# Optimization experiments

Measured on AMD Instinct MI355X. Metric: run time of the kernel, lower is better.

Reference implementation:

```python
import jax, jax.numpy as jnp
import numpy as np

NU, NI, NR = 50000, 50000, 5   # users, items, rating levels
D, B, LS, LI = 64, 512, 32, 64 # embed_dim, batch, max social nbrs, max item hist
NEG = -1e9


def setup_inputs() -> dict:
    key = jax.random.key(0)
    ks = iter(jax.random.split(key, 64))
    def lin(din, dout):
        s = 1.0 / np.sqrt(din)
        return (jax.random.uniform(next(ks), (din, dout), minval=-s, maxval=s, dtype=jnp.float32),
                jax.random.uniform(next(ks), (dout,), minval=-s, maxval=s, dtype=jnp.float32))
    inp = {}
    inp['user_w'] = jax.random.normal(next(ks), (NU, D), dtype=jnp.float32) * 0.1
    inp['item_w'] = jax.random.normal(next(ks), (NI, D), dtype=jnp.float32) * 0.1
    inp['rating_w'] = jax.random.normal(next(ks), (NR, D), dtype=jnp.float32) * 0.1
    for name, din, dout in [('i_ln1', 2*D, D), ('i_ln2', D, D), ('i_ln3', 2*D, D),
                            ('i_att1', 2*D, D), ('i_att2', D, D), ('i_att3', D, 1),
                            ('s_ln1', D, D), ('s_ln2', 2*D, D), ('s_ln3', D, D),
                            ('s_att1', 2*D, D), ('s_att2', D, D), ('s_att3', D, 1)]:
        w, b = lin(din, dout)
        inp[name + '_w'] = w
        inp[name + '_b'] = b
    inp['nodes'] = jax.random.randint(next(ks), (B,), 0, NU)
    inp['social_hist'] = jax.random.randint(next(ks), (NU, LS), 0, NU)
    inp['social_mask'] = jax.random.bernoulli(next(ks), 0.5, (NU, LS)).at[:, 0].set(True)
    inp['item_hist'] = jax.random.randint(next(ks), (NU, LI), 0, NI)
    inp['rating_hist'] = jax.random.randint(next(ks), (NU, LI), 0, NR)
    inp['item_mask'] = jax.random.bernoulli(next(ks), 0.5, (NU, LI)).at[:, 0].set(True)
    return inp


def reference(user_w, item_w, rating_w,
              i_ln1_w, i_ln1_b, i_ln2_w, i_ln2_b, i_ln3_w, i_ln3_b,
              i_att1_w, i_att1_b, i_att2_w, i_att2_b, i_att3_w, i_att3_b,
              s_ln1_w, s_ln1_b, s_ln2_w, s_ln2_b, s_ln3_w, s_ln3_b,
              s_att1_w, s_att1_b, s_att2_w, s_att2_b, s_att3_w, s_att3_b,
              nodes, social_hist, social_mask, item_hist, rating_hist, item_mask):
    relu = jax.nn.relu

    def attn(x, w1, b1, w2, b2, w3, b3, mask):
        # x: [..., L, 2D] -> softmax weights over valid neighbors: [..., L]
        h = relu(x @ w1 + b1)
        h = relu(h @ w2 + b2)
        logit = (h @ w3 + b3)[..., 0]
        logit = jnp.where(mask, logit, NEG)
        return jax.nn.softmax(logit, axis=-1)

    def item_final(uids):
        # uids: any shape [...]; returns [..., D]  (Aggre_item.item_final)
        its, rts, m = item_hist[uids], rating_hist[uids], item_mask[uids]
        x = jnp.concatenate([item_w[its], rating_w[rts]], axis=-1)   # [...,LI,2D]
        x = relu(x @ i_ln1_w + i_ln1_b)                              # [...,LI,D]
        u = user_w[uids]                                             # [...,D]
        a_in = jnp.concatenate([x, jnp.broadcast_to(u[..., None, :], x.shape)], axis=-1)
        alpha = attn(a_in, i_att1_w, i_att1_b, i_att2_w, i_att2_b, i_att3_w, i_att3_b, m)
        hI = jnp.einsum('...l,...ld->...d', alpha, x)                # attention-weighted sum
        hI = relu(hI @ i_ln2_w + i_ln2_b)
        return relu(jnp.concatenate([u, hI], axis=-1) @ i_ln3_w + i_ln3_b)

    # item-space factor of query users
    hI_self = item_final(nodes)                                      # [B,D]
    # social aggregation: item_final over each user's social neighbors
    nbrs, nmask = social_hist[nodes], social_mask[nodes]             # [B,LS]
    hI_nb = item_final(nbrs)                                         # [B,LS,D]
    u = user_w[nodes]                                                # [B,D]
    b_in = jnp.concatenate([hI_nb, jnp.broadcast_to(u[:, None, :], hI_nb.shape)], axis=-1)
    beta = attn(b_in, s_att1_w, s_att1_b, s_att2_w, s_att2_b, s_att3_w, s_att3_b, nmask)
    hS = jnp.einsum('bl,bld->bd', beta, hI_nb)
    hS = relu(hS @ s_ln1_w + s_ln1_b)
    f = jnp.concatenate([hI_self, hS], axis=-1)
    f = relu(f @ s_ln2_w + s_ln2_b)
    return relu(f @ s_ln3_w + s_ln3_b)
```

## Files before the change

kernel.cpp:

```cpp
#include <hip/hip_runtime.h>
#include <math.h>


#define NII 50000
#define BB 512
#define LSS 32
#define NT 16896

typedef short short8 __attribute__((ext_vector_type(8)));
typedef float f32x4 __attribute__((ext_vector_type(4)));

static __device__ __forceinline__ bool mread(const void* p, long i, int mode) {
  if (mode == 0) return ((const int*)p)[i] != 0;
  if (mode == 2) return ((const float*)p)[i] != 0.0f;
  return ((const unsigned char*)p)[i] != 0;
}

static __device__ __forceinline__ float wsum(float v) {
#pragma unroll
  for (int s = 1; s < 64; s <<= 1) v += __shfl_xor(v, s);
  return v;
}
static __device__ __forceinline__ float wmax(float v) {
#pragma unroll
  for (int s = 1; s < 64; s <<= 1) v = fmaxf(v, __shfl_xor(v, s));
  return v;
}
static __device__ __forceinline__ float rsum16(float v) {
#pragma unroll
  for (int s = 1; s < 16; s <<= 1) v += __shfl_xor(v, s);
  return v;
}

static __device__ __forceinline__ short bf16rne(float f) {
  unsigned u = __float_as_uint(f);
  u = (u + 0x7FFFu + ((u >> 16) & 1u)) >> 16;
  return (short)u;
}
static __device__ __forceinline__ float bf16tof(short h) {
  return __uint_as_float(((unsigned)(unsigned short)h) << 16);
}

static __device__ __forceinline__ void wave_fence() {
  asm volatile("s_waitcnt lgkmcnt(0)" ::: "memory");
  __builtin_amdgcn_sched_barrier(0);
}

__global__ void setup_kernel(const unsigned int* __restrict__ sm,
                             int* __restrict__ flag,
                             const float* __restrict__ rating_w,
                             const float* __restrict__ w1,
                             const float* __restrict__ b1,
                             float* __restrict__ RW1g,
                             const float* __restrict__ A1w,
                             const float* __restrict__ A2w,
                             short* __restrict__ B1,
                             short* __restrict__ B2,
                             short* __restrict__ W1hi,
                             short* __restrict__ W1lo,
                             const int* __restrict__ nodes,
                             const int* __restrict__ social_hist,
                             int* __restrict__ counter,
                             int* __restrict__ list,
                             int* __restrict__ aUid) {
  const int tid = threadIdx.x;
  if (blockIdx.x == 0) {
    __shared__ int notInt, notFloat;
    if (tid == 0) { notInt = 0; notFloat = 0; }
    __syncthreads();
    int ni = 0, nf = 0;
    for (int i = tid; i < 4096; i += 256) {
      unsigned int x = sm[i];
      if (x > 1u) ni = 1;
      if (x != 0u && x != 0x3F800000u) nf = 1;
    }
    if (ni) atomicOr(&notInt, 1);
    if (nf) atomicOr(&notFloat, 1);
    __syncthreads();
    if (tid == 0) flag[0] = notInt ? (notFloat ? 1 : 2) : 0;
  } else if (blockIdx.x == 1) {
    for (int t = tid; t < 320; t += 256) {
      const int r = t >> 6, c = t & 63;
      float acc = b1[c];
      for (int k = 0; k < 64; ++k)
        acc = fmaf(rating_w[r * 64 + k], w1[(64 + k) * 64 + c], acc);
      RW1g[r * 64 + c] = acc;
    }
  } else if (blockIdx.x == 2) {
    for (int idx = tid; idx < 4096; idx += 256) {
      int e = idx & 7, g = idx >> 3;
      int l = g & 63, q = g >> 6;
      int kb = q >> 2, nb = q & 3;
      int k = kb * 32 + ((l >> 4) & 3) * 8 + e;
      int col = nb * 16 + (l & 15);
      B1[idx] = bf16rne(A1w[k * 64 + col]);
      B2[idx] = bf16rne(A2w[k * 64 + col]);
      float a = w1[k * 64 + col];
      short h = bf16rne(a);
      W1hi[idx] = h;
      W1lo[idx] = bf16rne(a - bf16tof(h));
    }
  } else {
    __shared__ int nI, nF;
    if (tid == 0) { nI = 0; nF = 0; }
    __syncthreads();
    int ni = 0, nf = 0;
    for (int i = tid; i < 4096; i += 256) {
      unsigned int x = sm[i];
      if (x > 1u) ni = 1;
      if (x != 0u && x != 0x3F800000u) nf = 1;
    }
    if (ni) atomicOr(&nI, 1);
    if (nf) atomicOr(&nF, 1);
    __syncthreads();
    const int mode = nI ? (nF ? 1 : 2) : 0;
    const int t = (blockIdx.x - 3) * 256 + tid;
    if (t < NT) {
      int uid;
      bool active;
      if (t < BB) {
        active = true;
        uid = nodes[t];
      } else {
        int nb = t - BB;
        int b = nb >> 5, l = nb & 31;
        long mi = (long)nodes[b] * LSS + l;
        active = mread((const void*)sm, mi, mode);
        uid = active ? social_hist[mi] : 0;
      }
      if (active) {
        int pos = atomicAdd(counter, 1);
        list[pos] = t;
        aUid[pos] = uid;
      }
    }
  }
}

__global__ __launch_bounds__(256, 2)
void mid_kernel(const float* __restrict__ item_w,
                const short* __restrict__ W1hi,
                const short* __restrict__ W1lo,
                short* __restrict__ xbase16,
                const float* __restrict__ user_w,
                const float* __restrict__ A1w, const float* __restrict__ A1b,
                const int* __restrict__ aUid, const int* __restrict__ nActp,
                float* __restrict__ uA1buf) {
  const int tid = threadIdx.x, lane = tid & 63, w = tid >> 6;
  if (blockIdx.x < 512) {
    const int l15 = lane & 15, lg4 = lane >> 4;
    short8 bh[8], bl[8];
#pragma unroll
    for (int q = 0; q < 8; ++q) {
      bh[q] = *(const short8*)(W1hi + (q * 64 + lane) * 8);
      bl[q] = *(const short8*)(W1lo + (q * 64 + lane) * 8);
    }
    const int wid = blockIdx.x * 4 + w;
    for (int tile = wid; tile < 3125; tile += 2048) {
      const long r0 = (long)tile * 16;
      const float* ap = item_w + (r0 + l15) * 64 + lg4 * 8;
      short8 ah[2], al[2];
#pragma unroll
      for (int kb = 0; kb < 2; ++kb) {
        const float4 a = *(const float4*)(ap + kb * 32);
        const float4 b = *(const float4*)(ap + kb * 32 + 4);
        float v[8] = {a.x, a.y, a.z, a.w, b.x, b.y, b.z, b.w};
        short8 hi, lo;
#pragma unroll
        for (int e = 0; e < 8; ++e) {
          short h = bf16rne(v[e]);
          hi[e] = h;
          lo[e] = bf16rne(v[e] - bf16tof(h));
        }
        ah[kb] = hi;
        al[kb] = lo;
      }
#pragma unroll
      for (int nb = 0; nb < 4; ++nb) {
        f32x4 acc = {0.0f, 0.0f, 0.0f, 0.0f};
        acc = __builtin_amdgcn_mfma_f32_16x16x32_bf16(ah[0], bh[0 * 4 + nb], acc, 0, 0, 0);
        acc = __builtin_amdgcn_mfma_f32_16x16x32_bf16(ah[1], bh[1 * 4 + nb], acc, 0, 0, 0);
        acc = __builtin_amdgcn_mfma_f32_16x16x32_bf16(ah[0], bl[0 * 4 + nb], acc, 0, 0, 0);
        acc = __builtin_amdgcn_mfma_f32_16x16x32_bf16(ah[1], bl[1 * 4 + nb], acc, 0, 0, 0);
        acc = __builtin_amdgcn_mfma_f32_16x16x32_bf16(al[0], bh[0 * 4 + nb], acc, 0, 0, 0);
        acc = __builtin_amdgcn_mfma_f32_16x16x32_bf16(al[1], bh[1 * 4 + nb], acc, 0, 0, 0);
#pragma unroll
        for (int r = 0; r < 4; ++r)
          xbase16[(r0 + lg4 * 4 + r) * 64 + nb * 16 + l15] = bf16rne(acc[r]);
      }
    }
  } else {
    const int i0 = (blockIdx.x - 512) * 64;
    const int nA = nActp[0];
    if (i0 >= nA) return;
    __shared__ float sW[64][64], sU[64][64];
    __shared__ float sb[64];
    __shared__ int sUid[64];
    for (int i = tid; i < 4096; i += 256) sW[i >> 6][i & 63] = A1w[4096 + i];
    if (tid < 64) {
      sb[tid] = A1b[tid];
      sUid[tid] = (i0 + tid < nA) ? aUid[i0 + tid] : 0;
    }
    __syncthreads();
    for (int i = tid; i < 4096; i += 256) {
      int r = i >> 6, c = i & 63;
      sU[r][c] = user_w[(long)sUid[r] * 64 + c];
    }
    __syncthreads();
    float acc[16];
#pragma unroll
    for (int r = 0; r < 16; ++r) acc[r] = sb[lane];
    for (int k = 0; k < 64; k += 4) {
      float wv0 = sW[k][lane], wv1 = sW[k + 1][lane];
      float wv2 = sW[k + 2][lane], wv3 = sW[k + 3][lane];
#pragma unroll
      for (int r = 0; r < 16; ++r) {
        const float4 xv = *(const float4*)(&sU[w * 16 + r][k]);
        acc[r] = fmaf(xv.x, wv0, acc[r]);
        acc[r] = fmaf(xv.y, wv1, acc[r]);
        acc[r] = fmaf(xv.z, wv2, acc[r]);
        acc[r] = fmaf(xv.w, wv3, acc[r]);
      }
    }
#pragma unroll
    for (int r = 0; r < 16; ++r) {
      int row = i0 + w * 16 + r;
      if (row < nA) uA1buf[(long)row * 64 + lane] = acc[r];
    }
  }
}

__global__ __launch_bounds__(512, 8)
void core_mfma_kernel(const short* __restrict__ xb16,
                      const float* __restrict__ RW1g,
                      const float* __restrict__ uA1buf,
                      const short* __restrict__ Bimg1,
                      const short* __restrict__ Bimg2,
                      const float* __restrict__ A2b,
                      const float* __restrict__ A3w,
                      const int* __restrict__ item_hist,
                      const int* __restrict__ rating_hist,
                      const void* __restrict__ item_mask,
                      const int* __restrict__ flagp,
                      const int* __restrict__ aUid,
                      const int* __restrict__ nActp,
                      float* __restrict__ hvecbuf) {
  __shared__ __align__(16) short sB1[4096], sB2[4096];
  __shared__ __align__(16) char smem[8][3072];
  const int tid = threadIdx.x, lane = tid & 63, w = tid >> 6;
  const int nA = nActp[0];
  if (blockIdx.x * 8 >= nA) return;

  short* h1w = (short*)(smem[w]);
  float* lgw = (float*)(smem[w] + 2560);
  int* cw = (int*)(smem[w] + 2816);

  ((int4*)sB1)[tid] = ((const int4*)Bimg1)[tid];
  ((int4*)sB2)[tid] = ((const int4*)Bimg2)[tid];
  __syncthreads();

  const int idx = blockIdx.x * 8 + w;
  if (idx >= nA) return;

  const int mode = flagp[0];
  const float a2bv = A2b[lane];
  const float a3v = A3w[lane];
  const int l15 = lane & 15;
  const int lg4 = lane >> 4;

#define B1F(q) (*(const short8*)(sB1 + ((q) * 64 + lane) * 8))
#define B2F(q) (*(const short8*)(sB2 + ((q) * 64 + lane) * 8))

  const long uid = aUid[idx];

  const long mbase = uid * 64;
  bool mk = mread(item_mask, mbase + lane, mode);
  unsigned long long bal = __ballot(mk);
  const int nact = (int)__popcll(bal);
  int pos = (int)__popcll(bal & ((1ull << lane) - 1ull));
  if (mk) cw[pos] = (item_hist[mbase + lane] << 3) | rating_hist[mbase + lane];
  const float uA1v = uA1buf[(long)idx * 64 + lane];
  wave_fence();

  const int ng = (nact + 15) >> 4;
  for (int mc = 0; mc < ng; ++mc) {
    wave_fence();
    int row = mc * 16 + l15;
    if (row >= nact) row = nact - 1;
    const int p = cw[row];
    const long it = p >> 3;
    const int rt = p & 7;
    short8 xa[2];
#pragma unroll
    for (int kb = 0; kb < 2; ++kb) {
      const int koff = kb * 32 + lg4 * 8;
      const short8 xb = *(const short8*)(xb16 + it * 64 + koff);
      const float* rp = RW1g + rt * 64 + koff;
      const float4 c = *(const float4*)rp;
      const float4 d = *(const float4*)(rp + 4);
      short8 f;
      f[0] = bf16rne(fmaxf(bf16tof(xb[0]) + c.x, 0.0f));
      f[1] = bf16rne(fmaxf(bf16tof(xb[1]) + c.y, 0.0f));
      f[2] = bf16rne(fmaxf(bf16tof(xb[2]) + c.z, 0.0f));
      f[3] = bf16rne(fmaxf(bf16tof(xb[3]) + c.w, 0.0f));
      f[4] = bf16rne(fmaxf(bf16tof(xb[4]) + d.x, 0.0f));
      f[5] = bf16rne(fmaxf(bf16tof(xb[5]) + d.y, 0.0f));
      f[6] = bf16rne(fmaxf(bf16tof(xb[6]) + d.z, 0.0f));
      f[7] = bf16rne(fmaxf(bf16tof(xb[7]) + d.w, 0.0f));
      xa[kb] = f;
    }
#pragma unroll
    for (int nb = 0; nb < 4; ++nb) {
      const float ui = __shfl(uA1v, nb * 16 + l15);
      f32x4 acc = {ui, ui, ui, ui};
      acc = __builtin_amdgcn_mfma_f32_16x16x32_bf16(xa[0], B1F(0 * 4 + nb), acc, 0, 0, 0);
      acc = __builtin_amdgcn_mfma_f32_16x16x32_bf16(xa[1], B1F(1 * 4 + nb), acc, 0, 0, 0);
#pragma unroll
      for (int r = 0; r < 4; ++r)
        h1w[(lg4 * 4 + r) * 80 + nb * 16 + l15] = bf16rne(fmaxf(acc[r], 0.0f));
    }
    wave_fence();
    short8 ha[2];
    ha[0] = *(const short8*)(h1w + l15 * 80 + lg4 * 8);
    ha[1] = *(const short8*)(h1w + l15 * 80 + 32 + lg4 * 8);
    float t0 = 0.0f, t1 = 0.0f, t2 = 0.0f, t3 = 0.0f;
#pragma unroll
    for (int nb = 0; nb < 4; ++nb) {
      const float b2 = __shfl(a2bv, nb * 16 + l15);
      f32x4 acc = {b2, b2, b2, b2};
      acc = __builtin_amdgcn_mfma_f32_16x16x32_bf16(ha[0], B2F(0 * 4 + nb), acc, 0, 0, 0);
      acc = __builtin_amdgcn_mfma_f32_16x16x32_bf16(ha[1], B2F(1 * 4 + nb), acc, 0, 0, 0);
      const float a3c = __shfl(a3v, nb * 16 + l15);
      t0 = fmaf(fmaxf(acc[0], 0.0f), a3c, t0);
      t1 = fmaf(fmaxf(acc[1], 0.0f), a3c, t1);
      t2 = fmaf(fmaxf(acc[2], 0.0f), a3c, t2);
      t3 = fmaf(fmaxf(acc[3], 0.0f), a3c, t3);
    }
    t0 = rsum16(t0); t1 = rsum16(t1); t2 = rsum16(t2); t3 = rsum16(t3);
    if (l15 == 0) {
      const int jb = mc * 16 + lg4 * 4;
      lgw[jb + 0] = t0;
      lgw[jb + 1] = t1;
      lgw[jb + 2] = t2;
      lgw[jb + 3] = t3;
    }
  }
  wave_fence();

  const bool valid = (lane < nact);
  float lv = valid ? lgw[lane] : -1e30f;
  float mx = wmax(lv);
  float e = valid ? __expf(lv - mx) : 0.0f;
  float s = wsum(e);
  const float alpha = e / s;

  float h0 = 0.0f, hA = 0.0f, hB = 0.0f, hC = 0.0f;
  int j = 0;
  for (; j + 3 < nact; j += 4) {
    const int p0 = cw[j], p1 = cw[j + 1], p2 = cw[j + 2], p3 = cw[j + 3];
    const float a0 = __shfl(alpha, j), a1 = __shfl(alpha, j + 1);
    const float a2 = __shfl(alpha, j + 2), a3 = __shfl(alpha, j + 3);
    const float x0 = bf16tof(xb16[(long)(p0 >> 3) * 64 + lane]) + RW1g[(p0 & 7) * 64 + lane];
    const float x1 = bf16tof(xb16[(long)(p1 >> 3) * 64 + lane]) + RW1g[(p1 & 7) * 64 + lane];
    const float x2 = bf16tof(xb16[(long)(p2 >> 3) * 64 + lane]) + RW1g[(p2 & 7) * 64 + lane];
    const float x3 = bf16tof(xb16[(long)(p3 >> 3) * 64 + lane]) + RW1g[(p3 & 7) * 64 + lane];
    h0 = fmaf(a0, fmaxf(x0, 0.0f), h0);
    hA = fmaf(a1, fmaxf(x1, 0.0f), hA);
    hB = fmaf(a2, fmaxf(x2, 0.0f), hB);
    hC = fmaf(a3, fmaxf(x3, 0.0f), hC);
  }
  for (; j < nact; ++j) {
    const int p = cw[j];
    const float aj = __shfl(alpha, j);
    const float xv = bf16tof(xb16[(long)(p >> 3) * 64 + lane]) + RW1g[(p & 7) * 64 + lane];
    h0 = fmaf(aj, fmaxf(xv, 0.0f), h0);
  }
  hvecbuf[(long)idx * 64 + lane] = (h0 + hA) + (hB + hC);
#undef B1F
#undef B2F
}

__global__ __launch_bounds__(256, 2)
void hI2final_kernel(const float* __restrict__ hvecbuf,
                     const float* __restrict__ user_w,
                     const float* __restrict__ W2w, const float* __restrict__ W2b,
                     const float* __restrict__ W3w, const float* __restrict__ W3b,
                     const int* __restrict__ list, const int* __restrict__ aUid,
                     const int* __restrict__ nActp, float* __restrict__ hIbuf) {
  const int tid = threadIdx.x, lane = tid & 63, w = tid >> 6;
  const int i0 = blockIdx.x * 32;
  const int nA = nActp[0];
  if (i0 >= nA) return;
  __shared__ float sW[128][64];
  __shared__ float sX[32][128];
  __shared__ float sb[64];
  __shared__ int sUid[32], sInst[32];
  for (int i = tid; i < 4096; i += 256) sW[i >> 6][i & 63] = W2w[i];
  if (tid < 64) sb[tid] = W2b[tid];
  if (tid < 32) {
    bool ok = (i0 + tid) < nA;
    sUid[tid] = ok ? aUid[i0 + tid] : 0;
    sInst[tid] = ok ? list[i0 + tid] : 0;
  }
  __syncthreads();
  for (int i = tid; i < 2048; i += 256) {
    int r = i >> 6, c = i & 63;
    sX[r][64 + c] = (i0 + r < nA) ? hvecbuf[(long)(i0 + r) * 64 + c] : 0.0f;
    sX[r][c] = user_w[(long)sUid[r] * 64 + c];
  }
  __syncthreads();

  float acc[8];
  {
    const float bv = sb[lane];
#pragma unroll
    for (int r = 0; r < 8; ++r) acc[r] = bv;
    for (int k = 0; k < 64; k += 4) {
      float wv0 = sW[k][lane], wv1 = sW[k + 1][lane];
      float wv2 = sW[k + 2][lane], wv3 = sW[k + 3][lane];
#pragma unroll
      for (int r = 0; r < 8; ++r) {
        const float4 xv = *(const float4*)(&sX[w * 8 + r][64 + k]);
        acc[r] = fmaf(xv.x, wv0, acc[r]);
        acc[r] = fmaf(xv.y, wv1, acc[r]);
        acc[r] = fmaf(xv.z, wv2, acc[r]);
        acc[r] = fmaf(xv.w, wv3, acc[r]);
      }
    }
#pragma unroll
    for (int r = 0; r < 8; ++r) sX[w * 8 + r][64 + lane] = fmaxf(acc[r], 0.0f);
  }
  __syncthreads();
  for (int i = tid; i < 8192; i += 256) sW[i >> 6][i & 63] = W3w[i];
  if (tid < 64) sb[tid] = W3b[tid];
  __syncthreads();

  {
    const float bv = sb[lane];
#pragma unroll
    for (int r = 0; r < 8; ++r) acc[r] = bv;
    for (int k = 0; k < 128; k += 4) {
      float wv0 = sW[k][lane], wv1 = sW[k + 1][lane];
      float wv2 = sW[k + 2][lane], wv3 = sW[k + 3][lane];
#pragma unroll
      for (int r = 0; r < 8; ++r) {
        const float4 xv = *(const float4*)(&sX[w * 8 + r][k]);
        acc[r] = fmaf(xv.x, wv0, acc[r]);
        acc[r] = fmaf(xv.y, wv1, acc[r]);
        acc[r] = fmaf(xv.z, wv2, acc[r]);
        acc[r] = fmaf(xv.w, wv3, acc[r]);
      }
    }
#pragma unroll
    for (int r = 0; r < 8; ++r) {
      int row = i0 + w * 8 + r;
      if (row < nA)
        hIbuf[(long)sInst[w * 8 + r] * 64 + lane] = fmaxf(acc[r], 0.0f);
    }
  }
}

__global__ __launch_bounds__(256, 8)
void social_fused_kernel(const float* __restrict__ hIbuf,
                         const float* __restrict__ user_w,
                         const float* __restrict__ S1w,
                         const float* __restrict__ S1b,
                         const float* __restrict__ S2w,
                         const float* __restrict__ S2b,
                         const float* __restrict__ S3w,
                         const float* __restrict__ L1w, const float* __restrict__ L1b,
                         const float* __restrict__ L2w, const float* __restrict__ L2b,
                         const float* __restrict__ L3w, const float* __restrict__ L3b,
                         const int* __restrict__ nodes,
                         const void* __restrict__ social_mask,
                         const int* __restrict__ flagp,
                         float* __restrict__ out) {
  __shared__ __align__(16) short sB1[4096], sB2[4096];
  __shared__ __align__(16) char smem[4][3584];
  const int tid = threadIdx.x, lane = tid & 63, w = tid >> 6;
  short* h1w = (short*)(smem[w]);
  float* lgw = (float*)(smem[w] + 2560);
  int* cw = (int*)(smem[w] + 2816);
  float* vA = (float*)(smem[w] + 3072);
  float* vB = (float*)(smem[w] + 3328);

  for (int i = tid; i < 4096; i += 256) {
    int e = i & 7, g = i >> 3;
    int l = g & 63, q = g >> 6;
    int kb = q >> 2, nb = q & 3;
    int k = kb * 32 + ((l >> 4) & 3) * 8 + e;
    int col = nb * 16 + (l & 15);
    sB1[i] = bf16rne(S1w[k * 64 + col]);
    sB2[i] = bf16rne(S2w[k * 64 + col]);
  }
  __syncthreads();

  const int mode = flagp[0];
  const int l15 = lane & 15;
  const int lg4 = lane >> 4;
  const int b = blockIdx.x * 4 + w;
  const long uid = nodes[b];

  bool m = (lane < LSS) ? mread(social_mask, uid * LSS + lane, mode) : false;
  unsigned long long bal = __ballot(m);
  const int nval = (int)__popcll(bal);
  int pos = (int)__popcll(bal & ((1ull << lane) - 1ull));
  if (m) cw[pos] = lane;

  const float uv = user_w[uid * 64 + lane];
  float uA1v = S1b[lane];
#pragma unroll 8
  for (int k = 0; k < 64; ++k)
    uA1v = fmaf(__shfl(uv, k), S1w[(64 + k) * 64 + lane], uA1v);
  const float a2bv = S2b[lane];
  const float a3v = S3w[lane];
  wave_fence();

  const long hbase = 512L + (long)b * 32;
  const int ng = (nval + 15) >> 4;
  for (int mc = 0; mc < ng; ++mc) {
    wave_fence();
    int row = mc * 16 + l15;
    if (row >= nval) row = nval - 1;
    const long hrow = hbase + cw[row];
    short8 xa[2];
#pragma unroll
    for (int kb = 0; kb < 2; ++kb) {
      const float* xp = hIbuf + hrow * 64 + kb * 32 + lg4 * 8;
      const float4 a = *(const float4*)xp;
      const float4 bb = *(const float4*)(xp + 4);
      short8 f;
      f[0] = bf16rne(a.x);  f[1] = bf16rne(a.y);
      f[2] = bf16rne(a.z);  f[3] = bf16rne(a.w);
      f[4] = bf16rne(bb.x); f[5] = bf16rne(bb.y);
      f[6] = bf16rne(bb.z); f[7] = bf16rne(bb.w);
      xa[kb] = f;
    }
#pragma unroll
    for (int nb = 0; nb < 4; ++nb) {
      const float ui = __shfl(uA1v, nb * 16 + l15);
      f32x4 acc = {ui, ui, ui, ui};
      acc = __builtin_amdgcn_mfma_f32_16x16x32_bf16(
          xa[0], *(const short8*)(sB1 + ((0 * 4 + nb) * 64 + lane) * 8), acc, 0, 0, 0);
      acc = __builtin_amdgcn_mfma_f32_16x16x32_bf16(
          xa[1], *(const short8*)(sB1 + ((1 * 4 + nb) * 64 + lane) * 8), acc, 0, 0, 0);
#pragma unroll
      for (int r = 0; r < 4; ++r)
        h1w[(lg4 * 4 + r) * 80 + nb * 16 + l15] = bf16rne(fmaxf(acc[r], 0.0f));
    }
    wave_fence();
    short8 ha[2];
    ha[0] = *(const short8*)(h1w + l15 * 80 + lg4 * 8);
    ha[1] = *(const short8*)(h1w + l15 * 80 + 32 + lg4 * 8);
    float t0 = 0.0f, t1 = 0.0f, t2 = 0.0f, t3 = 0.0f;
#pragma unroll
    for (int nb = 0; nb < 4; ++nb) {
      const float b2 = __shfl(a2bv, nb * 16 + l15);
      f32x4 acc = {b2, b2, b2, b2};
      acc = __builtin_amdgcn_mfma_f32_16x16x32_bf16(
          ha[0], *(const short8*)(sB2 + ((0 * 4 + nb) * 64 + lane) * 8), acc, 0, 0, 0);
      acc = __builtin_amdgcn_mfma_f32_16x16x32_bf16(
          ha[1], *(const short8*)(sB2 + ((1 * 4 + nb) * 64 + lane) * 8), acc, 0, 0, 0);
      const float a3c = __shfl(a3v, nb * 16 + l15);
      t0 = fmaf(fmaxf(acc[0], 0.0f), a3c, t0);
      t1 = fmaf(fmaxf(acc[1], 0.0f), a3c, t1);
      t2 = fmaf(fmaxf(acc[2], 0.0f), a3c, t2);
      t3 = fmaf(fmaxf(acc[3], 0.0f), a3c, t3);
    }
    t0 = rsum16(t0); t1 = rsum16(t1); t2 = rsum16(t2); t3 = rsum16(t3);
    if (l15 == 0) {
      const int jb = mc * 16 + lg4 * 4;
      lgw[jb + 0] = t0;
      lgw[jb + 1] = t1;
      lgw[jb + 2] = t2;
      lgw[jb + 3] = t3;
    }
  }
  wave_fence();

  const bool valid = (lane < nval);
  float lv = valid ? lgw[lane] : -1e30f;
  float mx = wmax(lv);
  float e = valid ? __expf(lv - mx) : 0.0f;
  float s = wsum(e);
  const float beta = e / s;

  float hs = 0.0f;
  for (int j = 0; j < nval; ++j) {
    const float bj = __shfl(beta, j);
    hs = fmaf(bj, hIbuf[(hbase + cw[j]) * 64 + lane], hs);
  }

  vA[lane] = hs;
  wave_fence();
  float acc = L1b[lane];
#pragma unroll 8
  for (int k = 0; k < 64; ++k) acc = fmaf(vA[k], L1w[k * 64 + lane], acc);
  const float vecB = fmaxf(acc, 0.0f);
  const float selfv = hIbuf[(long)b * 64 + lane];
  wave_fence();
  vA[lane] = selfv;
  vB[lane] = vecB;
  wave_fence();
  acc = L2b[lane];
#pragma unroll 8
  for (int k = 0; k < 64; ++k) acc = fmaf(vA[k], L2w[k * 64 + lane], acc);
#pragma unroll 8
  for (int k = 0; k < 64; ++k) acc = fmaf(vB[k], L2w[(64 + k) * 64 + lane], acc);
  const float fv = fmaxf(acc, 0.0f);
  wave_fence();
  vA[lane] = fv;
  wave_fence();
  acc = L3b[lane];
#pragma unroll 8
  for (int k = 0; k < 64; ++k) acc = fmaf(vA[k], L3w[k * 64 + lane], acc);
  out[(long)b * 64 + lane] = fmaxf(acc, 0.0f);
}

extern "C" void kernel_launch(void* const* d_in, const int* in_sizes, int n_in,
                              void* d_out, int out_size, void* d_ws, size_t ws_size,
                              hipStream_t stream) {
  const float* user_w   = (const float*)d_in[0];
  const float* item_w   = (const float*)d_in[1];
  const float* rating_w = (const float*)d_in[2];
  const float* i_ln1_w  = (const float*)d_in[3];
  const float* i_ln1_b  = (const float*)d_in[4];
  const float* i_ln2_w  = (const float*)d_in[5];
  const float* i_ln2_b  = (const float*)d_in[6];
  const float* i_ln3_w  = (const float*)d_in[7];
  const float* i_ln3_b  = (const float*)d_in[8];
  const float* i_att1_w = (const float*)d_in[9];
  const float* i_att1_b = (const float*)d_in[10];
  const float* i_att2_w = (const float*)d_in[11];
  const float* i_att2_b = (const float*)d_in[12];
  const float* i_att3_w = (const float*)d_in[13];
  const float* i_att3_b = (const float*)d_in[14];
  const float* s_ln1_w  = (const float*)d_in[15];
  const float* s_ln1_b  = (const float*)d_in[16];
  const float* s_ln2_w  = (const float*)d_in[17];
  const float* s_ln2_b  = (const float*)d_in[18];
  const float* s_ln3_w  = (const float*)d_in[19];
  const float* s_ln3_b  = (const float*)d_in[20];
  const float* s_att1_w = (const float*)d_in[21];
  const float* s_att1_b = (const float*)d_in[22];
  const float* s_att2_w = (const float*)d_in[23];
  const float* s_att2_b = (const float*)d_in[24];
  const float* s_att3_w = (const float*)d_in[25];
  const float* s_att3_b = (const float*)d_in[26];
  const int*  nodes       = (const int*)d_in[27];
  const int*  social_hist = (const int*)d_in[28];
  const void* social_mask = d_in[29];
  const int*  item_hist   = (const int*)d_in[30];
  const int*  rating_hist = (const int*)d_in[31];
  const void* item_mask   = d_in[32];

  char* ws = (char*)d_ws;
  int*   flag    = (int*)(ws + 0);
  int*   counter = (int*)(ws + 256);
  int*   list    = (int*)(ws + 512);
  int*   aUid    = (int*)(ws + 68096);
  float* uA1buf  = (float*)(ws + 135680);
  float* hIbuf   = uA1buf;
  float* hvecbuf = (float*)(ws + 4461056);
  short* W1hi    = (short*)(ws + 4461056);
  short* W1lo    = (short*)(ws + 4469248);
  short* xbase16 = (short*)(ws + 8786432);
  float* RW1g    = (float*)(ws + 21586432);
  short* Bimg1   = (short*)(ws + 21587712);
  short* Bimg2   = (short*)(ws + 21595904);

  hipMemsetAsync(counter, 0, 4, stream);
  setup_kernel<<<3 + NT / 256, 256, 0, stream>>>(
      (const unsigned int*)social_mask, flag,
      rating_w, i_ln1_w, i_ln1_b, RW1g,
      i_att1_w, i_att2_w, Bimg1, Bimg2, W1hi, W1lo,
      nodes, social_hist, counter, list, aUid);
  mid_kernel<<<512 + NT / 64, 256, 0, stream>>>(
      item_w, W1hi, W1lo, xbase16,
      user_w, i_att1_w, i_att1_b, aUid, counter, uA1buf);
  core_mfma_kernel<<<NT / 8, 512, 0, stream>>>(
      xbase16, RW1g, uA1buf, Bimg1, Bimg2, i_att2_b, i_att3_w,
      item_hist, rating_hist, item_mask, flag, aUid, counter, hvecbuf);
  hI2final_kernel<<<NT / 32, 256, 0, stream>>>(
      hvecbuf, user_w, i_ln2_w, i_ln2_b, i_ln3_w, i_ln3_b,
      list, aUid, counter, hIbuf);
  social_fused_kernel<<<BB / 4, 256, 0, stream>>>(
      hIbuf, user_w, s_att1_w, s_att1_b, s_att2_w, s_att2_b, s_att3_w,
      s_ln1_w, s_ln1_b, s_ln2_w, s_ln2_b, s_ln3_w, s_ln3_b,
      nodes, social_mask, flag, (float*)d_out);
}
```

Before: 105.9 us.

## Replace atomic active-instance compaction with direct dense instance indexing

Drops the atomic-counter compaction of active (query + masked social neighbor) instances, along with the memset and the extra setup blocks. Each downstream kernel now derives its user id directly from nodes/social_hist using the dense instance index. uA1 and hI2final run for every slot, including inactive ones, and core_mfma skips inactive slots via a mask check. This removes a launch-side memset, the atomics and a level of indirection, at the cost of extra work on masked-out neighbors in the dense kernels.

```diff
diff --git a/kernel.cpp b/kernel.cpp
--- a/kernel.cpp
+++ b/kernel.cpp
@@ -44,6 +44,22 @@
 static __device__ __forceinline__ void wave_fence() {
   asm volatile("s_waitcnt lgkmcnt(0)" ::: "memory");
   __builtin_amdgcn_sched_barrier(0);
+}
+
+static __device__ __forceinline__ bool inst_uid(int t, const int* nodes,
+                                                const int* social_hist,
+                                                const void* social_mask,
+                                                int mode, long* uid) {
+  if (t < BB) {
+    *uid = nodes[t];
+    return true;
+  }
+  const int nb = t - BB;
+  const int b = nb >> 5, l = nb & 31;
+  const long mi = (long)nodes[b] * LSS + l;
+  if (!mread(social_mask, mi, mode)) return false;
+  *uid = social_hist[mi];
+  return true;
 }
 
 __global__ void setup_kernel(const unsigned int* __restrict__ sm,
@@ -57,12 +73,7 @@
                              short* __restrict__ B1,
                              short* __restrict__ B2,
                              short* __restrict__ W1hi,
-                             short* __restrict__ W1lo,
-                             const int* __restrict__ nodes,
-                             const int* __restrict__ social_hist,
-                             int* __restrict__ counter,
-                             int* __restrict__ list,
-                             int* __restrict__ aUid) {
+                             short* __restrict__ W1lo) {
   const int tid = threadIdx.x;
   if (blockIdx.x == 0) {
     __shared__ int notInt, notFloat;
@@ -86,7 +97,7 @@
         acc = fmaf(rating_w[r * 64 + k], w1[(64 + k) * 64 + c], acc);
       RW1g[r * 64 + c] = acc;
     }
-  } else if (blockIdx.x == 2) {
+  } else {
     for (int idx = tid; idx < 4096; idx += 256) {
       int e = idx & 7, g = idx >> 3;
       int l = g & 63, q = g >> 6;
@@ -100,40 +111,6 @@
       W1hi[idx] = h;
       W1lo[idx] = bf16rne(a - bf16tof(h));
     }
-  } else {
-    __shared__ int nI, nF;
-    if (tid == 0) { nI = 0; nF = 0; }
-    __syncthreads();
-    int ni = 0, nf = 0;
-    for (int i = tid; i < 4096; i += 256) {
-      unsigned int x = sm[i];
-      if (x > 1u) ni = 1;
-      if (x != 0u && x != 0x3F800000u) nf = 1;
-    }
-    if (ni) atomicOr(&nI, 1);
-    if (nf) atomicOr(&nF, 1);
-    __syncthreads();
-    const int mode = nI ? (nF ? 1 : 2) : 0;
-    const int t = (blockIdx.x - 3) * 256 + tid;
-    if (t < NT) {
-      int uid;
-      bool active;
-      if (t < BB) {
-        active = true;
-        uid = nodes[t];
-      } else {
-        int nb = t - BB;
-        int b = nb >> 5, l = nb & 31;
-        long mi = (long)nodes[b] * LSS + l;
-        active = mread((const void*)sm, mi, mode);
-        uid = active ? social_hist[mi] : 0;
-      }
-      if (active) {
-        int pos = atomicAdd(counter, 1);
-        list[pos] = t;
-        aUid[pos] = uid;
-      }
-    }
   }
 }
 
@@ -144,7 +121,8 @@
                 short* __restrict__ xbase16,
                 const float* __restrict__ user_w,
                 const float* __restrict__ A1w, const float* __restrict__ A1b,
-                const int* __restrict__ aUid, const int* __restrict__ nActp,
+                const int* __restrict__ nodes,
+                const int* __restrict__ social_hist,
                 float* __restrict__ uA1buf) {
   const int tid = threadIdx.x, lane = tid & 63, w = tid >> 6;
   if (blockIdx.x < 512) {
@@ -191,15 +169,21 @@
     }
   } else {
     const int i0 = (blockIdx.x - 512) * 64;
-    const int nA = nActp[0];
-    if (i0 >= nA) return;
     __shared__ float sW[64][64], sU[64][64];
     __shared__ float sb[64];
     __shared__ int sUid[64];
     for (int i = tid; i < 4096; i += 256) sW[i >> 6][i & 63] = A1w[4096 + i];
     if (tid < 64) {
       sb[tid] = A1b[tid];
-      sUid[tid] = (i0 + tid < nA) ? aUid[i0 + tid] : 0;
+      const int t = i0 + tid;
+      int uid;
+      if (t < BB) {
+        uid = nodes[t];
+      } else {
+        const int nb = t - BB;
+        uid = social_hist[(long)nodes[nb >> 5] * LSS + (nb & 31)];
+      }
+      sUid[tid] = uid;
     }
     __syncthreads();
     for (int i = tid; i < 4096; i += 256) {
@@ -223,10 +207,8 @@
       }
     }
 #pragma unroll
-    for (int r = 0; r < 16; ++r) {
-      int row = i0 + w * 16 + r;
-      if (row < nA) uA1buf[(long)row * 64 + lane] = acc[r];
-    }
+    for (int r = 0; r < 16; ++r)
+      uA1buf[(long)(i0 + w * 16 + r) * 64 + lane] = acc[r];
   }
 }
 
@@ -242,14 +224,13 @@
                       const int* __restrict__ rating_hist,
                       const void* __restrict__ item_mask,
                       const int* __restrict__ flagp,
-                      const int* __restrict__ aUid,
-                      const int* __restrict__ nActp,
+                      const int* __restrict__ nodes,
+                      const int* __restrict__ social_hist,
+                      const void* __restrict__ social_mask,
                       float* __restrict__ hvecbuf) {
   __shared__ __align__(16) short sB1[4096], sB2[4096];
   __shared__ __align__(16) char smem[8][3072];
   const int tid = threadIdx.x, lane = tid & 63, w = tid >> 6;
-  const int nA = nActp[0];
-  if (blockIdx.x * 8 >= nA) return;
 
   short* h1w = (short*)(smem[w]);
   float* lgw = (float*)(smem[w] + 2560);
@@ -259,10 +240,12 @@
   ((int4*)sB2)[tid] = ((const int4*)Bimg2)[tid];
   __syncthreads();
 
-  const int idx = blockIdx.x * 8 + w;
-  if (idx >= nA) return;
-
+  const int t = blockIdx.x * 8 + w;
   const int mode = flagp[0];
+  long uid;
+  if (!inst_uid(t, nodes, social_hist, social_mask, mode, &uid))
+    return;
+
   const float a2bv = A2b[lane];
   const float a3v = A3w[lane];
   const int l15 = lane & 15;
@@ -270,8 +253,6 @@
 
 #define B1F(q) (*(const short8*)(sB1 + ((q) * 64 + lane) * 8))
 #define B2F(q) (*(const short8*)(sB2 + ((q) * 64 + lane) * 8))
-
-  const long uid = aUid[idx];
 
   const long mbase = uid * 64;
   bool mk = mread(item_mask, mbase + lane, mode);
@@ -279,7 +260,7 @@
   const int nact = (int)__popcll(bal);
   int pos = (int)__popcll(bal & ((1ull << lane) - 1ull));
   if (mk) cw[pos] = (item_hist[mbase + lane] << 3) | rating_hist[mbase + lane];
-  const float uA1v = uA1buf[(long)idx * 64 + lane];
+  const float uA1v = uA1buf[(long)t * 64 + lane];
   wave_fence();
 
   const int ng = (nact + 15) >> 4;
@@ -375,7 +356,7 @@
     const float xv = bf16tof(xb16[(long)(p >> 3) * 64 + lane]) + RW1g[(p & 7) * 64 + lane];
     h0 = fmaf(aj, fmaxf(xv, 0.0f), h0);
   }
-  hvecbuf[(long)idx * 64 + lane] = (h0 + hA) + (hB + hC);
+  hvecbuf[(long)t * 64 + lane] = (h0 + hA) + (hB + hC);
 #undef B1F
 #undef B2F
 }
@@ -385,27 +366,32 @@
                      const float* __restrict__ user_w,
                      const float* __restrict__ W2w, const float* __restrict__ W2b,
                      const float* __restrict__ W3w, const float* __restrict__ W3b,
-                     const int* __restrict__ list, const int* __restrict__ aUid,
-                     const int* __restrict__ nActp, float* __restrict__ hIbuf) {
+                     const int* __restrict__ nodes,
+                     const int* __restrict__ social_hist,
+                     float* __restrict__ hIbuf) {
   const int tid = threadIdx.x, lane = tid & 63, w = tid >> 6;
   const int i0 = blockIdx.x * 32;
-  const int nA = nActp[0];
-  if (i0 >= nA) return;
   __shared__ float sW[128][64];
   __shared__ float sX[32][128];
   __shared__ float sb[64];
-  __shared__ int sUid[32], sInst[32];
+  __shared__ int sUid[32];
   for (int i = tid; i < 4096; i += 256) sW[i >> 6][i & 63] = W2w[i];
   if (tid < 64) sb[tid] = W2b[tid];
   if (tid < 32) {
-    bool ok = (i0 + tid) < nA;
-    sUid[tid] = ok ? aUid[i0 + tid] : 0;
-    sInst[tid] = ok ? list[i0 + tid] : 0;
+    const int t = i0 + tid;
+    int uid;
+    if (t < BB) {
+      uid = nodes[t];
+    } else {
+      const int nb = t - BB;
+      uid = social_hist[(long)nodes[nb >> 5] * LSS + (nb & 31)];
+    }
+    sUid[tid] = uid;
   }
   __syncthreads();
   for (int i = tid; i < 2048; i += 256) {
     int r = i >> 6, c = i & 63;
-    sX[r][64 + c] = (i0 + r < nA) ? hvecbuf[(long)(i0 + r) * 64 + c] : 0.0f;
+    sX[r][64 + c] = hvecbuf[(long)(i0 + r) * 64 + c];
     sX[r][c] = user_w[(long)sUid[r] * 64 + c];
   }
   __syncthreads();
@@ -452,11 +438,8 @@
       }
     }
 #pragma unroll
-    for (int r = 0; r < 8; ++r) {
-      int row = i0 + w * 8 + r;
-      if (row < nA)
-        hIbuf[(long)sInst[w * 8 + r] * 64 + lane] = fmaxf(acc[r], 0.0f);
-    }
+    for (int r = 0; r < 8; ++r)
+      hIbuf[(long)(i0 + w * 8 + r) * 64 + lane] = fmaxf(acc[r], 0.0f);
   }
 }
 
@@ -656,9 +639,6 @@
 
   char* ws = (char*)d_ws;
   int*   flag    = (int*)(ws + 0);
-  int*   counter = (int*)(ws + 256);
-  int*   list    = (int*)(ws + 512);
-  int*   aUid    = (int*)(ws + 68096);
   float* uA1buf  = (float*)(ws + 135680);
   float* hIbuf   = uA1buf;
   float* hvecbuf = (float*)(ws + 4461056);
@@ -669,21 +649,20 @@
   short* Bimg1   = (short*)(ws + 21587712);
   short* Bimg2   = (short*)(ws + 21595904);
 
-  hipMemsetAsync(counter, 0, 4, stream);
-  setup_kernel<<<3 + NT / 256, 256, 0, stream>>>(
+  setup_kernel<<<3, 256, 0, stream>>>(
       (const unsigned int*)social_mask, flag,
       rating_w, i_ln1_w, i_ln1_b, RW1g,
-      i_att1_w, i_att2_w, Bimg1, Bimg2, W1hi, W1lo,
-      nodes, social_hist, counter, list, aUid);
+      i_att1_w, i_att2_w, Bimg1, Bimg2, W1hi, W1lo);
   mid_kernel<<<512 + NT / 64, 256, 0, stream>>>(
       item_w, W1hi, W1lo, xbase16,
-      user_w, i_att1_w, i_att1_b, aUid, counter, uA1buf);
+      user_w, i_att1_w, i_att1_b, nodes, social_hist, uA1buf);
   core_mfma_kernel<<<NT / 8, 512, 0, stream>>>(
       xbase16, RW1g, uA1buf, Bimg1, Bimg2, i_att2_b, i_att3_w,
-      item_hist, rating_hist, item_mask, flag, aUid, counter, hvecbuf);
+      item_hist, rating_hist, item_mask, flag,
+      nodes, social_hist, social_mask, hvecbuf);
   hI2final_kernel<<<NT / 32, 256, 0, stream>>>(
       hvecbuf, user_w, i_ln2_w, i_ln2_b, i_ln3_w, i_ln3_b,
-      list, aUid, counter, hIbuf);
+      nodes, social_hist, hIbuf);
   social_fused_kernel<<<BB / 4, 256, 0, stream>>>(
       hIbuf, user_w, s_att1_w, s_att1_b, s_att2_w, s_att2_b, s_att3_w,
       s_ln1_w, s_ln1_b, s_ln2_w, s_ln2_b, s_ln3_w, s_ln3_b,
```

New measurement: 107.8 us. About the same (+1.8%).
